# Optimization experiments

Measured on AMD Instinct MI355X. Metric: run time of the kernel, lower is better.

The kernel has to match this reference:

```python
import jax, jax.numpy as jnp
import numpy as np
from jax.scipy.special import gammaln

BLOCK = 96          # NIQE block size at scale 1 (48 at scale 2)
KSIZE = 7           # gaussian MSCN window size
SIGMA = 7.0 / 6.0   # gaussian sigma
PAD = KSIZE // 2
NUM_FEAT = 18       # features per block per scale

# gamma grid for AGGD shape-parameter search (matches torch.arange(0.2, 10.001, 0.001))
AGGD_GRID = jnp.asarray(np.arange(0.2, 10.0 + 0.001, 0.001), dtype=jnp.float32)
R_GAM = jnp.exp(2.0 * gammaln(2.0 / AGGD_GRID) - (gammaln(1.0 / AGGD_GRID) + gammaln(3.0 / AGGD_GRID)))


def _gauss_kernel():
    m = (KSIZE - 1) / 2.0
    y, x = np.ogrid[-m:m + 1, -m:m + 1]
    h = np.exp(-(x * x + y * y) / (2.0 * SIGMA * SIGMA))
    h[h < np.finfo(h.dtype).eps * h.max()] = 0
    h = h / h.sum()
    return jnp.asarray(h, dtype=jnp.float32)[None, None]  # (1,1,7,7)

GAUSS = _gauss_kernel()


def imfilter(x):
    # replicate ('same') padding + valid conv, like _image_filter
    xp = jnp.pad(x, ((0, 0), (0, 0), (PAD, PAD), (PAD, PAD)), mode='edge')
    return jax.lax.conv_general_dilated(xp, GAUSS, (1, 1), 'VALID')


def estimate_aggd(blocks):
    # blocks: (N, k, k)
    mask_l = blocks < 0
    mask_r = blocks > 0
    cl = jnp.sum(mask_l, axis=(-1, -2)).astype(blocks.dtype)
    cr = jnp.sum(mask_r, axis=(-1, -2)).astype(blocks.dtype)
    left_std = jnp.sqrt(jnp.sum(jnp.where(mask_l, blocks, 0.0) ** 2, axis=(-1, -2)) / (cl + 1e-8))
    right_std = jnp.sqrt(jnp.sum(jnp.where(mask_r, blocks, 0.0) ** 2, axis=(-1, -2)) / (cr + 1e-8))
    gamma_hat = left_std / right_std
    rhat = jnp.mean(jnp.abs(blocks), axis=(-1, -2)) ** 2 / jnp.mean(blocks ** 2, axis=(-1, -2))
    rhat_norm = rhat * (gamma_hat ** 3 + 1.0) * (gamma_hat + 1.0) / (gamma_hat ** 2 + 1.0) ** 2
    pos = jnp.argmin(jnp.abs(R_GAM[None, :] - rhat_norm[:, None]), axis=-1)  # (N, 9801) search
    alpha = AGGD_GRID[pos]
    conv = jnp.sqrt(jnp.exp(gammaln(1.0 / alpha) - gammaln(3.0 / alpha)))
    return alpha, left_std * conv, right_std * conv


def mscn_features(blocks):
    # blocks: (N, k, k) -> (N, 18)
    alpha, lb, rb = estimate_aggd(blocks)
    feats = [alpha, (lb + rb) / 2.0]
    for sh in ((0, 1), (1, 0), (1, 1), (1, -1)):
        shifted = jnp.roll(blocks, sh, axis=(-2, -1))
        a, l, r = estimate_aggd(blocks * shifted)
        mean = (r - l) * jnp.exp(gammaln(2.0 / a) - gammaln(1.0 / a))
        feats.extend((a, mean, l, r))
    return jnp.stack(feats, axis=-1)


def blockify(img, bs):
    # img: (b,1,H,W) -> (b, nb, bs, bs); partial blocks discarded like _blockproc_torch
    b, _, h, w = img.shape
    nbh, nbw = h // bs, w // bs
    x = img[:, 0, :nbh * bs, :nbw * bs].reshape(b, nbh, bs, nbw, bs)
    return x.transpose(0, 1, 3, 2, 4).reshape(b, nbh * nbw, bs, bs)


def mscn_normalize(img):
    mu = imfilter(img)
    sigma = jnp.sqrt(jnp.abs(imfilter(img * img) - mu * mu))
    return (img - mu) / (sigma + 1.0)


def niqe_score(image, mu_pris, cov_pris):
    img = image
    feats = []
    for scale in (1, 2):
        norm = mscn_normalize(img)
        blocks = blockify(norm, BLOCK // scale)
        b, nb, k, _ = blocks.shape
        f = mscn_features(blocks.reshape(b * nb, k, k)).reshape(b, nb, NUM_FEAT)
        feats.append(f)
        if scale == 1:
            # 2x2 average-pool downsample for second scale
            bb, cc, hh, ww = img.shape
            img = img.reshape(bb, cc, hh // 2, 2, ww // 2, 2).mean(axis=(3, 5))
    feats = jnp.concatenate(feats, axis=-1)  # (b, nb, 36)
    nb = feats.shape[1]
    mu_dist = feats.mean(axis=1)                        # (b, 36)
    xm = feats - mu_dist[:, None, :]
    cov_dist = jnp.einsum('bnf,bng->bfg', xm, xm) / (nb - 1)
    cov = (cov_pris[None] + cov_dist) / 2.0
    diff = mu_pris[None, :] - mu_dist                   # (b, 36)
    invc = jnp.linalg.pinv(cov)
    quad = jnp.einsum('bf,bfg,bg->b', diff, invc, diff)
    return jnp.sqrt(jnp.maximum(quad, 0.0))


def setup_inputs() -> dict:
    key = jax.random.key(0)
    k1, k2, k3 = jax.random.split(key, 3)
    image = jax.random.uniform(k1, (16, 1, 1056, 1056), dtype=jnp.float32)
    mu_pris = jax.random.normal(k2, (36,), dtype=jnp.float32)
    a = jax.random.normal(k3, (36, 36), dtype=jnp.float32)
    cov_pris = a @ a.T / 36.0 + 0.5 * jnp.eye(36, dtype=jnp.float32)  # SPD pristine covariance
    return {'image': image, 'mu_pris': mu_pris, 'cov_pris': cov_pris}


def reference(image, mu_pris, cov_pris):
    return niqe_score(image, mu_pris, cov_pris)
```

## Files before the change

### kernel.cpp

```cpp
#include <hip/hip_runtime.h>
#include <math.h>

#define NGRID 9801
#define NB 11
#define NBLK (NB*NB)
#define BATCH 16
#define NFEAT 36

__global__ void init_tables(float* __restrict__ rgam, float* __restrict__ convt,
                            float* __restrict__ meanf, float* __restrict__ w1d) {
    int i = blockIdx.x * blockDim.x + threadIdx.x;
    if (i < NGRID) {
        double a = (double)(float)(0.2 + 0.001 * (double)i);
        double g1 = lgamma(1.0 / a);
        double g2 = lgamma(2.0 / a);
        double g3 = lgamma(3.0 / a);
        rgam[i]  = (float)exp(2.0 * g2 - g1 - g3);
        convt[i] = (float)sqrt(exp(g1 - g3));
        meanf[i] = (float)exp(g2 - g1);
    }
    if (i == 0) {
        double g[7], s = 0.0;
        for (int k = 0; k < 7; ++k) { double d = (double)(k - 3); g[k] = exp(-d * d * 18.0 / 49.0); s += g[k]; }
        for (int k = 0; k < 7; ++k) w1d[k] = (float)(g[k] / s);
    }
}

__device__ __forceinline__ float bperm(int addr, float v) {
    return __int_as_float(__builtin_amdgcn_ds_bpermute(addr, __float_as_int(v)));
}

template <int K, bool WDS>
__global__ __launch_bounds__(256) void fused_mscn_stats(
        const float* __restrict__ img, float* __restrict__ dsout,
        const float* __restrict__ w1d, float* __restrict__ stats) {
    constexpr int NSLAB = K / 48;
    constexpr int NSTRIP = 4 / NSLAB;
    constexpr int SROWS = K / NSTRIP;
    constexpr int W = K * NB;
    constexpr int H = W;

    __shared__ float lastrow[NSTRIP][K];
    __shared__ float edgeL[NSTRIP][NSLAB][SROWS];
    __shared__ float edgeR[NSTRIP][NSLAB][SROWS];
    __shared__ float redf[4][15];
    __shared__ float redc[4][10];

    const int tid = threadIdx.x;
    const int lane = tid & 63;
    const int wv = tid >> 6;
    const int slab = wv % NSLAB;
    const int strip = wv / NSLAB;
    const int bIdx = blockIdx.x;
    const int b = blockIdx.y;
    const int bh = bIdx / NB, bw = bIdx % NB;
    const int x0 = bw * K + slab * 48;
    const int gx = x0 - 3 + lane;
    const int gxc = min(max(gx, 0), W - 1);
    const int r0 = bh * K + strip * SROWS;
    const int basem3 = (lane - 3) << 2;
    const bool act = (lane >= 3) && (lane <= 50);
    int am1, ap1;
    if constexpr (NSLAB == 1) {
        am1 = ((lane == 3) ? 50 : (lane - 1)) << 2;
        ap1 = ((lane == 50) ? 3 : (lane + 1)) << 2;
    } else {
        am1 = ((lane - 1) & 63) << 2;
        ap1 = ((lane + 1) & 63) << 2;
    }

    const float* im = img + (size_t)b * H * W + gxc;
    const float w0=w1d[0], w1=w1d[1], w2=w1d[2], w3=w1d[3], w4=w1d[4], w5=w1d[5], w6=w1d[6];

    auto ld = [&](int r) -> float {
        int rc = min(max(r, 0), H - 1);
        return im[(size_t)rc * W];
    };

    float pa0, pa1, pa2, pa4, pa5, pa6, vHp;
    auto issue_raw = [&](float v) {
        pa0 = bperm(basem3,      v);
        pa1 = bperm(basem3 + 4,  v);
        pa2 = bperm(basem3 + 8,  v);
        pa4 = bperm(basem3 + 16, v);
        pa5 = bperm(basem3 + 20, v);
        pa6 = bperm(basem3 + 24, v);
        vHp = v;
    };
    auto combine_raw = [&](float& om, float& oq) {
        om = ((w0*pa0 + w1*pa1) + (w2*pa2 + w3*vHp)) + ((w4*pa4 + w5*pa5) + w6*pa6);
        oq = ((w0*pa0*pa0 + w1*pa1*pa1) + (w2*pa2*pa2 + w3*vHp*vHp))
           + ((w4*pa4*pa4 + w5*pa5*pa5) + w6*pa6*pa6);
    };

    float acc[5][3];
    #pragma unroll
    for (int s = 0; s < 5; ++s) { acc[s][0] = acc[s][1] = acc[s][2] = 0.f; }
    int cl[5] = {0,0,0,0,0}, cr[5] = {0,0,0,0,0};

    auto upd = [&](int s, float v) {
        float vp = fmaxf(v, 0.f);
        acc[s][0] = fmaf(vp, vp, acc[s][0]);
        acc[s][1] = fmaf(v, v, acc[s][1]);
        acc[s][2] += fabsf(v);
        cl[s] += __popcll(__ballot(v < 0.f));
        cr[s] += __popcll(__ballot(v > 0.f));
    };

    float mr0,mr1,mr2,mr3,mr4,mr5,mr6, qr0,qr1,qr2,qr3,qr4,qr5,qr6;
    float rA, rB, rC, rD;
    float vN = ld(r0 - 3);
    { float v=vN; vN=ld(r0-2); issue_raw(v); combine_raw(mr0,qr0); }
    { float v=vN; vN=ld(r0-1); issue_raw(v); combine_raw(mr1,qr1); }
    { float v=vN; vN=ld(r0+0); issue_raw(v); combine_raw(mr2,qr2); }
    { float v=vN; vN=ld(r0+1); issue_raw(v); combine_raw(mr3,qr3); rA=v; }
    { float v=vN; vN=ld(r0+2); issue_raw(v); combine_raw(mr4,qr4); rB=v; }
    { float v=vN; vN=ld(r0+3); issue_raw(v); combine_raw(mr5,qr5); rC=v; }
    { float v=vN; vN=ld(r0+4); issue_raw(v); combine_raw(mr6,qr6); rD=v; }
    { float v=vN; vN=ld(r0+5); issue_raw(v); }

    float normP = 0.f, normP2 = 0.f;
    float pendSL = 0.f, pendPL = 0.f, pendPR = 0.f;
    float firstN = 0.f, dsSave = 0.f;
    const bool dsw = WDS && (lane & 1) && (lane >= 3) && (lane <= 49);

    #pragma unroll 4
    for (int yy = 0; yy < SROWS; ++yy) {
        const int y = r0 + yy;
        if (yy > 0) {
            upd(0, normP);
            upd(1, normP * pendSL);
            upd(2, normP * normP2);
            upd(3, normP * pendPL);
            upd(4, normP * pendPR);
        }
        float mu = ((w0*mr0 + w1*mr1) + (w2*mr2 + w3*mr3)) + ((w4*mr4 + w5*mr5) + w6*mr6);
        float s2 = ((w0*qr0 + w1*qr1) + (w2*qr2 + w3*qr3)) + ((w4*qr4 + w5*qr5) + w6*qr6);
        float sig = __builtin_amdgcn_sqrtf(fabsf(s2 - mu * mu));
        float nrm = (rA - mu) * __builtin_amdgcn_rcpf(sig + 1.0f);
        float cur = act ? nrm : 0.f;

        if (yy == 0) firstN = cur;
        if constexpr (NSLAB == 2) {
            if (lane == 3)  edgeL[strip][slab][yy] = cur;
            if (lane == 50) edgeR[strip][slab][yy] = cur;
        }
        if (yy == SROWS - 1 && act) lastrow[strip][slab * 48 + lane - 3] = cur;

        if constexpr (WDS) {
            float hs = rA + __shfl_down(rA, 1);
            if ((y & 1) == 0) dsSave = hs;
            else if (dsw)
                dsout[((size_t)b * (H / 2) + (y >> 1)) * (W / 2) + (gx >> 1)] = 0.25f * (dsSave + hs);
        }

        pendSL = bperm(am1, cur);
        pendPL = bperm(am1, normP);
        pendPR = bperm(ap1, normP);
        normP2 = normP; normP = cur;

        float mh, qh; combine_raw(mh, qh);
        mr0=mr1; mr1=mr2; mr2=mr3; mr3=mr4; mr4=mr5; mr5=mr6; mr6=mh;
        qr0=qr1; qr1=qr2; qr2=qr3; qr3=qr4; qr4=qr5; qr5=qr6; qr6=qh;

        rA=rB; rB=rC; rC=rD; rD=vHp;
        float vv = vN; vN = ld(y + 6);
        issue_raw(vv);
    }
    upd(0, normP);
    upd(1, normP * pendSL);
    upd(2, normP * normP2);
    upd(3, normP * pendPL);
    upd(4, normP * pendPR);

    __syncthreads();

    {
        const int ps = (strip + NSTRIP - 1) % NSTRIP;
        int j  = slab * 48 + (lane - 3);
        int js = act ? j : 0;
        int jm1 = (js + K - 1) % K;
        int jp1 = (js + 1) % K;
        float pv  = act ? lastrow[ps][js]  : 0.f;
        float pvL = act ? lastrow[ps][jm1] : 0.f;
        float pvR = act ? lastrow[ps][jp1] : 0.f;
        upd(2, firstN * pv);
        upd(3, firstN * pvL);
        upd(4, firstN * pvR);
    }

    if constexpr (NSLAB == 2) {
        if (lane < SROWS) {
            int r = lane;
            if (slab == 0) {
                float c0  = edgeL[strip][0][r];
                float e95 = edgeR[strip][1][r];
                upd(1, c0 * e95);
                if (r > 0) {
                    upd(3, c0 * edgeR[strip][1][r - 1]);
                    upd(4, edgeR[strip][0][r] * edgeL[strip][1][r - 1]);
                }
            } else {
                float c48 = edgeL[strip][1][r];
                float e47 = edgeR[strip][0][r];
                upd(1, c48 * e47);
                if (r > 0) {
                    upd(3, c48 * edgeR[strip][0][r - 1]);
                    upd(4, edgeR[strip][1][r] * edgeL[strip][0][r - 1]);
                }
            }
        }
    }

    #pragma unroll
    for (int off = 32; off >= 1; off >>= 1)
        #pragma unroll
        for (int s = 0; s < 5; ++s) {
            acc[s][0] += __shfl_down(acc[s][0], off);
            acc[s][1] += __shfl_down(acc[s][1], off);
            acc[s][2] += __shfl_down(acc[s][2], off);
        }
    if (lane == 0) {
        #pragma unroll
        for (int s = 0; s < 5; ++s) {
            redf[wv][s*3+0] = acc[s][0];
            redf[wv][s*3+1] = acc[s][1];
            redf[wv][s*3+2] = acc[s][2];
            redc[wv][s*2+0] = (float)cl[s];
            redc[wv][s*2+1] = (float)cr[s];
        }
    }
    __syncthreads();
    if (tid < 15) {
        stats[((size_t)b * NBLK + bIdx) * 25 + tid] =
            redf[0][tid] + redf[1][tid] + redf[2][tid] + redf[3][tid];
    } else if (tid < 25) {
        int t = tid - 15;
        stats[((size_t)b * NBLK + bIdx) * 25 + tid] =
            redc[0][t] + redc[1][t] + redc[2][t] + redc[3][t];
    }
}

__global__ __launch_bounds__(256) void aggd_kernel(
        const float* __restrict__ stats1, const float* __restrict__ stats2,
        const float* __restrict__ rgam, const float* __restrict__ convt,
        const float* __restrict__ meanf, float* __restrict__ feats) {
    __shared__ float rg[NGRID];
    for (int i = threadIdx.x; i < NGRID; i += 256) rg[i] = rgam[i];
    __syncthreads();

    int gid = blockIdx.x * 256 + threadIdx.x;
    if (gid >= 2 * BATCH * NBLK * 5) return;
    int s = gid % 5; int t = gid / 5;
    int blk = t % NBLK; t /= NBLK;
    int b = t % BATCH; int scale = t / BATCH;

    const float* st = (scale ? stats2 : stats1) + ((size_t)b * NBLK + blk) * 25;
    float sr2 = st[s*3+0], ssq = st[s*3+1], sab = st[s*3+2];
    float cl = st[15 + 2*s], cr = st[15 + 2*s + 1];
    float sl2 = fmaxf(ssq - sr2, 0.f);
    float n = scale ? (48.f * 48.f) : (96.f * 96.f);

    float lstd = sqrtf(sl2 / (cl + 1e-8f));
    float rstd = sqrtf(sr2 / (cr + 1e-8f));
    float gh = lstd / rstd;
    float mab = sab / n;
    float msq = ssq / n;
    float rhat = mab * mab / msq;
    float g2 = gh * gh;
    float x = rhat * (gh * g2 + 1.f) * (gh + 1.f) / ((g2 + 1.f) * (g2 + 1.f));

    int lo = 0, hi = NGRID;
    while (lo < hi) {
        int mid = (lo + hi) >> 1;
        if (rg[mid] < x) lo = mid + 1; else hi = mid;
    }
    int gi;
    if (lo <= 0) gi = 0;
    else if (lo >= NGRID) gi = NGRID - 1;
    else {
        float dlo = x - rg[lo - 1];
        float dhi = rg[lo] - x;
        gi = (dlo <= dhi) ? lo - 1 : lo;
    }

    float alpha = (float)(0.2 + 0.001 * (double)gi);
    float cv = convt[gi];
    float lb = lstd * cv, rb = rstd * cv;
    float* fo = feats + ((size_t)b * NBLK + blk) * NFEAT + (scale ? 18 : 0);
    if (s == 0) {
        fo[0] = alpha;
        fo[1] = 0.5f * (lb + rb);
    } else {
        int o = 2 + (s - 1) * 4;
        fo[o]     = alpha;
        fo[o + 1] = (rb - lb) * meanf[gi];
        fo[o + 2] = lb;
        fo[o + 3] = rb;
    }
}

__global__ __launch_bounds__(256) void score_kernel(
        const float* __restrict__ feats, const float* __restrict__ mu_pris,
        const float* __restrict__ cov_pris, float* __restrict__ out) {
    __shared__ float F[NBLK][NFEAT];
    __shared__ double mu[NFEAT];
    __shared__ double A[NFEAT][NFEAT + 1];
    __shared__ double dff[NFEAT];
    __shared__ double xs[NFEAT];
    int b = blockIdx.x, tid = threadIdx.x;
    const float* fp = feats + (size_t)b * NBLK * NFEAT;
    for (int i = tid; i < NBLK * NFEAT; i += 256) F[i / NFEAT][i % NFEAT] = fp[i];
    __syncthreads();
    if (tid < NFEAT) {
        double s = 0.0;
        for (int n = 0; n < NBLK; ++n) s += (double)F[n][tid];
        mu[tid] = s / (double)NBLK;
        dff[tid] = (double)mu_pris[tid] - mu[tid];
    }
    __syncthreads();
    for (int e = tid; e < NFEAT * NFEAT; e += 256) {
        int f = e / NFEAT, g = e % NFEAT;
        double mf = mu[f], mg = mu[g];
        double s = 0.0;
        for (int n = 0; n < NBLK; ++n) s += ((double)F[n][f] - mf) * ((double)F[n][g] - mg);
        A[f][g] = (s / (double)(NBLK - 1) + (double)cov_pris[f * NFEAT + g]) * 0.5;
    }
    if (tid < NFEAT) A[tid][NFEAT] = dff[tid];
    for (int k = 0; k < NFEAT - 1; ++k) {
        __syncthreads();
        double rk = 1.0 / A[k][k];
        for (int e = tid; e < NFEAT * (NFEAT + 1); e += 256) {
            int r = e / (NFEAT + 1), c = e % (NFEAT + 1);
            if (r > k && c > k) A[r][c] -= (A[r][k] * rk) * A[k][c];
        }
    }
    __syncthreads();
    for (int i = NFEAT - 1; i >= 0; --i) {
        if (tid == i) xs[i] = A[i][NFEAT] / A[i][i];
        __syncthreads();
        if (tid < i) A[tid][NFEAT] -= A[tid][i] * xs[i];
    }
    __syncthreads();
    if (tid == 0) {
        double quad = 0.0;
        for (int i = 0; i < NFEAT; ++i) quad += dff[i] * xs[i];
        out[b] = (float)sqrt(fmax(quad, 0.0));
    }
}

extern "C" void kernel_launch(void* const* d_in, const int* in_sizes, int n_in,
                              void* d_out, int out_size, void* d_ws, size_t ws_size,
                              hipStream_t stream) {
    const float* img      = (const float*)d_in[0];
    const float* mu_pris  = (const float*)d_in[1];
    const float* cov_pris = (const float*)d_in[2];
    float* out = (float*)d_out;
    float* ws = (float*)d_ws;

    float* rgam  = ws;
    float* convt = rgam + 9856;
    float* meanf = convt + 9856;
    float* w1d   = meanf + 9856;
    float* stats1 = w1d + 8;
    float* stats2 = stats1 + BATCH * NBLK * 25;
    float* feats  = stats2 + BATCH * NBLK * 25;
    float* dsimg  = feats + BATCH * NBLK * NFEAT;

    init_tables<<<(NGRID + 255) / 256, 256, 0, stream>>>(rgam, convt, meanf, w1d);

    fused_mscn_stats<96, true><<<dim3(NBLK, BATCH), 256, 0, stream>>>(
        img, dsimg, w1d, stats1);
    fused_mscn_stats<48, false><<<dim3(NBLK, BATCH), 256, 0, stream>>>(
        dsimg, nullptr, w1d, stats2);

    aggd_kernel<<<(2 * BATCH * NBLK * 5 + 255) / 256, 256, 0, stream>>>(
        stats1, stats2, rgam, convt, meanf, feats);

    score_kernel<<<BATCH, 256, 0, stream>>>(feats, mu_pris, cov_pris, out);
}
```

Measured before the change: 178.1 us.

## Use DPP lane shifts, packed v2f math and deeper row prefetch in MSCN stats

Replaces the ds_bpermute-based horizontal 7-tap neighbour gathers and the neighbour products with chained DPP wave_shr/wave_shl shifts, which avoid the LDS crossbar. Mean and second-moment filtering and the accumulators are packed into two-wide float vectors so the compiler can emit packed FMAs. Row loads now use an incrementing byte offset with edge clamping, and the prefetch queue is deepened to four rows ahead. The aim is lower per-row latency and instruction count, at the cost of more live registers and reliance on the edge-lane zero fill from DPP bound control.

```diff
diff --git a/kernel.cpp b/kernel.cpp
--- a/kernel.cpp
+++ b/kernel.cpp
@@ -6,6 +6,8 @@
 #define NBLK (NB*NB)
 #define BATCH 16
 #define NFEAT 36
+
+typedef float v2f __attribute__((ext_vector_type(2)));
 
 __global__ void init_tables(float* __restrict__ rgam, float* __restrict__ convt,
                             float* __restrict__ meanf, float* __restrict__ w1d) {
@@ -28,6 +30,14 @@
 
 __device__ __forceinline__ float bperm(int addr, float v) {
     return __int_as_float(__builtin_amdgcn_ds_bpermute(addr, __float_as_int(v)));
+}
+__device__ __forceinline__ float dpp_getL(float v) {
+    return __int_as_float(__builtin_amdgcn_update_dpp(
+        0, __float_as_int(v), 0x138 , 0xF, 0xF, true));
+}
+__device__ __forceinline__ float dpp_getR(float v) {
+    return __int_as_float(__builtin_amdgcn_update_dpp(
+        0, __float_as_int(v), 0x130 , 0xF, 0xF, true));
 }
 
 template <int K, bool WDS>
@@ -58,66 +68,76 @@
     const int gx = x0 - 3 + lane;
     const int gxc = min(max(gx, 0), W - 1);
     const int r0 = bh * K + strip * SROWS;
-    const int basem3 = (lane - 3) << 2;
     const bool act = (lane >= 3) && (lane <= 50);
-    int am1, ap1;
+    int am1 = 0, ap1 = 0;
     if constexpr (NSLAB == 1) {
         am1 = ((lane == 3) ? 50 : (lane - 1)) << 2;
         ap1 = ((lane == 50) ? 3 : (lane + 1)) << 2;
-    } else {
-        am1 = ((lane - 1) & 63) << 2;
-        ap1 = ((lane + 1) & 63) << 2;
-    }
-
-    const float* im = img + (size_t)b * H * W + gxc;
+    }
+
+    const char* baseB = (const char*)(img + (size_t)b * H * W);
     const float w0=w1d[0], w1=w1d[1], w2=w1d[2], w3=w1d[3], w4=w1d[4], w5=w1d[5], w6=w1d[6];
 
-    auto ld = [&](int r) -> float {
-        int rc = min(max(r, 0), H - 1);
-        return im[(size_t)rc * W];
+    int addrB = (min(max(r0 - 3, 0), H - 1) * W + gxc) * 4;
+    int rowNext = r0 - 2;
+    auto ld = [&]() -> float {
+        float v = *(const float*)(baseB + addrB);
+        addrB += (rowNext >= 1 && rowNext < H) ? (W * 4) : 0;
+        ++rowNext;
+        return v;
     };
 
     float pa0, pa1, pa2, pa4, pa5, pa6, vHp;
     auto issue_raw = [&](float v) {
-        pa0 = bperm(basem3,      v);
-        pa1 = bperm(basem3 + 4,  v);
-        pa2 = bperm(basem3 + 8,  v);
-        pa4 = bperm(basem3 + 16, v);
-        pa5 = bperm(basem3 + 20, v);
-        pa6 = bperm(basem3 + 24, v);
+        pa2 = dpp_getL(v);
+        pa1 = dpp_getL(pa2);
+        pa0 = dpp_getL(pa1);
+        pa4 = dpp_getR(v);
+        pa5 = dpp_getR(pa4);
+        pa6 = dpp_getR(pa5);
         vHp = v;
     };
-    auto combine_raw = [&](float& om, float& oq) {
-        om = ((w0*pa0 + w1*pa1) + (w2*pa2 + w3*vHp)) + ((w4*pa4 + w5*pa5) + w6*pa6);
-        oq = ((w0*pa0*pa0 + w1*pa1*pa1) + (w2*pa2*pa2 + w3*vHp*vHp))
-           + ((w4*pa4*pa4 + w5*pa5*pa5) + w6*pa6*pa6);
+    auto sq2 = [](float v) -> v2f { v2f t; t.x = v; t.y = v * v; return t; };
+    auto combine_raw = [&]() -> v2f {
+        v2f r = sq2(pa0) * w0;
+        r += sq2(pa1) * w1;
+        r += sq2(pa2) * w2;
+        r += sq2(vHp) * w3;
+        r += sq2(pa4) * w4;
+        r += sq2(pa5) * w5;
+        r += sq2(pa6) * w6;
+        return r;
     };
 
-    float acc[5][3];
+    v2f accp[5];
+    float sab[5];
     #pragma unroll
-    for (int s = 0; s < 5; ++s) { acc[s][0] = acc[s][1] = acc[s][2] = 0.f; }
+    for (int s = 0; s < 5; ++s) { accp[s] = (v2f)0.f; sab[s] = 0.f; }
     int cl[5] = {0,0,0,0,0}, cr[5] = {0,0,0,0,0};
 
     auto upd = [&](int s, float v) {
         float vp = fmaxf(v, 0.f);
-        acc[s][0] = fmaf(vp, vp, acc[s][0]);
-        acc[s][1] = fmaf(v, v, acc[s][1]);
-        acc[s][2] += fabsf(v);
+        v2f t; t.x = vp; t.y = v;
+        accp[s] += t * t;
+        sab[s] += fabsf(v);
         cl[s] += __popcll(__ballot(v < 0.f));
         cr[s] += __popcll(__ballot(v > 0.f));
     };
 
-    float mr0,mr1,mr2,mr3,mr4,mr5,mr6, qr0,qr1,qr2,qr3,qr4,qr5,qr6;
+    v2f mq0,mq1,mq2,mq3,mq4,mq5,mq6;
     float rA, rB, rC, rD;
-    float vN = ld(r0 - 3);
-    { float v=vN; vN=ld(r0-2); issue_raw(v); combine_raw(mr0,qr0); }
-    { float v=vN; vN=ld(r0-1); issue_raw(v); combine_raw(mr1,qr1); }
-    { float v=vN; vN=ld(r0+0); issue_raw(v); combine_raw(mr2,qr2); }
-    { float v=vN; vN=ld(r0+1); issue_raw(v); combine_raw(mr3,qr3); rA=v; }
-    { float v=vN; vN=ld(r0+2); issue_raw(v); combine_raw(mr4,qr4); rB=v; }
-    { float v=vN; vN=ld(r0+3); issue_raw(v); combine_raw(mr5,qr5); rC=v; }
-    { float v=vN; vN=ld(r0+4); issue_raw(v); combine_raw(mr6,qr6); rD=v; }
-    { float v=vN; vN=ld(r0+5); issue_raw(v); }
+    float vN = ld();
+    { float v=vN; vN=ld(); issue_raw(v); mq0=combine_raw(); }
+    { float v=vN; vN=ld(); issue_raw(v); mq1=combine_raw(); }
+    { float v=vN; vN=ld(); issue_raw(v); mq2=combine_raw(); }
+    { float v=vN; vN=ld(); issue_raw(v); mq3=combine_raw(); rA=v; }
+    { float v=vN; vN=ld(); issue_raw(v); mq4=combine_raw(); rB=v; }
+    { float v=vN; vN=ld(); issue_raw(v); mq5=combine_raw(); rC=v; }
+    { float v=vN; vN=ld(); issue_raw(v); mq6=combine_raw(); rD=v; }
+    { float v=vN; vN=ld(); issue_raw(v); }
+    float vN2 = ld();
+    float vN3 = ld();
+    float vN4 = ld();
 
     float normP = 0.f, normP2 = 0.f;
     float pendSL = 0.f, pendPL = 0.f, pendPR = 0.f;
@@ -134,8 +154,14 @@
             upd(3, normP * pendPL);
             upd(4, normP * pendPR);
         }
-        float mu = ((w0*mr0 + w1*mr1) + (w2*mr2 + w3*mr3)) + ((w4*mr4 + w5*mr5) + w6*mr6);
-        float s2 = ((w0*qr0 + w1*qr1) + (w2*qr2 + w3*qr3)) + ((w4*qr4 + w5*qr5) + w6*qr6);
+        v2f ms = mq0 * w0;
+        ms += mq1 * w1;
+        ms += mq2 * w2;
+        ms += mq3 * w3;
+        ms += mq4 * w4;
+        ms += mq5 * w5;
+        ms += mq6 * w6;
+        float mu = ms.x, s2 = ms.y;
         float sig = __builtin_amdgcn_sqrtf(fabsf(s2 - mu * mu));
         float nrm = (rA - mu) * __builtin_amdgcn_rcpf(sig + 1.0f);
         float cur = act ? nrm : 0.f;
@@ -148,23 +174,28 @@
         if (yy == SROWS - 1 && act) lastrow[strip][slab * 48 + lane - 3] = cur;
 
         if constexpr (WDS) {
-            float hs = rA + __shfl_down(rA, 1);
+            float hs = rA + dpp_getR(rA);
             if ((y & 1) == 0) dsSave = hs;
             else if (dsw)
                 dsout[((size_t)b * (H / 2) + (y >> 1)) * (W / 2) + (gx >> 1)] = 0.25f * (dsSave + hs);
         }
 
-        pendSL = bperm(am1, cur);
-        pendPL = bperm(am1, normP);
-        pendPR = bperm(ap1, normP);
+        if constexpr (NSLAB == 2) {
+            pendSL = dpp_getL(cur);
+            pendPL = dpp_getL(normP);
+            pendPR = dpp_getR(normP);
+        } else {
+            pendSL = bperm(am1, cur);
+            pendPL = bperm(am1, normP);
+            pendPR = bperm(ap1, normP);
+        }
         normP2 = normP; normP = cur;
 
-        float mh, qh; combine_raw(mh, qh);
-        mr0=mr1; mr1=mr2; mr2=mr3; mr3=mr4; mr4=mr5; mr5=mr6; mr6=mh;
-        qr0=qr1; qr1=qr2; qr2=qr3; qr3=qr4; qr4=qr5; qr5=qr6; qr6=qh;
+        v2f mh = combine_raw();
+        mq0=mq1; mq1=mq2; mq2=mq3; mq3=mq4; mq4=mq5; mq5=mq6; mq6=mh;
 
         rA=rB; rB=rC; rC=rD; rD=vHp;
-        float vv = vN; vN = ld(y + 6);
+        float vv = vN; vN=vN2; vN2=vN3; vN3=vN4; vN4=ld();
         issue_raw(vv);
     }
     upd(0, normP);
@@ -216,16 +247,16 @@
     for (int off = 32; off >= 1; off >>= 1)
         #pragma unroll
         for (int s = 0; s < 5; ++s) {
-            acc[s][0] += __shfl_down(acc[s][0], off);
-            acc[s][1] += __shfl_down(acc[s][1], off);
-            acc[s][2] += __shfl_down(acc[s][2], off);
+            accp[s].x += __shfl_down(accp[s].x, off);
+            accp[s].y += __shfl_down(accp[s].y, off);
+            sab[s]    += __shfl_down(sab[s],    off);
         }
     if (lane == 0) {
         #pragma unroll
         for (int s = 0; s < 5; ++s) {
-            redf[wv][s*3+0] = acc[s][0];
-            redf[wv][s*3+1] = acc[s][1];
-            redf[wv][s*3+2] = acc[s][2];
+            redf[wv][s*3+0] = accp[s].x;
+            redf[wv][s*3+1] = accp[s].y;
+            redf[wv][s*3+2] = sab[s];
             redc[wv][s*2+0] = (float)cl[s];
             redc[wv][s*2+1] = (float)cr[s];
         }
```

Result: faster. 157.8 us (median of 2 runs) (-11.4%).
